# Kernel tuning notes

Measured on AMD Instinct MI355X. Metric: run time of the kernel, lower is better.

The kernel has to match this reference:

```python
import jax, jax.numpy as jnp
import numpy as np

N_NODES = 100000
N_EDGES = 1000000
NEG_SLOPE = 0.2


def gat_conv(x, src, dst, W, al, ar, b, res, activation):
    """DGL-style GATConv. res is None (no residual), 'id' (identity residual), or a [in,H*D] matrix."""
    H, D = al.shape
    n = x.shape[0]
    feat = (x @ W).reshape(n, H, D)                      # [N,H,D]
    el = jnp.einsum('nhd,hd->nh', feat, al)              # [N,H]
    er = jnp.einsum('nhd,hd->nh', feat, ar)              # [N,H]
    e = jax.nn.leaky_relu(el[src] + er[dst], NEG_SLOPE)  # [E,H]
    # edge softmax over incoming edges of each dst node
    m = jax.lax.stop_gradient(jax.ops.segment_max(e, dst, num_segments=n))
    ex = jnp.exp(e - m[dst])
    s = jax.ops.segment_sum(ex, dst, num_segments=n)
    alpha = ex / s[dst]                                  # [E,H]
    out = jax.ops.segment_sum(feat[src] * alpha[:, :, None], dst, num_segments=n)  # [N,H,D]
    if res == 'id':
        out = out + x.reshape(n, H, D)
    elif res is not None:
        out = out + (x @ res).reshape(n, H, D)
    out = out + b.reshape(1, H, D)
    if activation is not None:
        out = activation(out)
    return out


def setup_inputs() -> dict:
    key = jax.random.key(0)
    ks = jax.random.split(key, 20)
    F_IN, HID = 128, 32
    H1, H2, H3 = 4, 4, 1
    C = 40
    sc = 0.1
    inp = {
        'x':   jax.random.normal(ks[0], (N_NODES, F_IN), dtype=jnp.float32),
        'src': jax.random.randint(ks[1], (N_EDGES,), 0, N_NODES, dtype=jnp.int32),
        'dst': jax.random.randint(ks[2], (N_EDGES,), 0, N_NODES, dtype=jnp.int32),
        # layer 1: in=128 -> H1*HID=128, no residual, elu
        'W1':  sc * jax.random.normal(ks[3], (F_IN, H1 * HID), dtype=jnp.float32),
        'al1': sc * jax.random.normal(ks[4], (H1, HID), dtype=jnp.float32),
        'ar1': sc * jax.random.normal(ks[5], (H1, HID), dtype=jnp.float32),
        'b1':  jnp.zeros((H1 * HID,), dtype=jnp.float32),
        # layer 2: in=128 -> H2*HID=128, identity residual, elu
        'W2':  sc * jax.random.normal(ks[6], (H1 * HID, H2 * HID), dtype=jnp.float32),
        'al2': sc * jax.random.normal(ks[7], (H2, HID), dtype=jnp.float32),
        'ar2': sc * jax.random.normal(ks[8], (H2, HID), dtype=jnp.float32),
        'b2':  jnp.zeros((H2 * HID,), dtype=jnp.float32),
        # layer 3 (output): in=128 -> H3*HID=32, projected residual, no activation
        'W3':  sc * jax.random.normal(ks[9], (H2 * HID, H3 * HID), dtype=jnp.float32),
        'al3': sc * jax.random.normal(ks[10], (H3, HID), dtype=jnp.float32),
        'ar3': sc * jax.random.normal(ks[11], (H3, HID), dtype=jnp.float32),
        'b3':  jnp.zeros((H3 * HID,), dtype=jnp.float32),
        'res3': sc * jax.random.normal(ks[12], (H2 * HID, H3 * HID), dtype=jnp.float32),
        # final classifier
        'Wfc': sc * jax.random.normal(ks[13], (HID, C), dtype=jnp.float32),
        'bfc': jnp.zeros((C,), dtype=jnp.float32),
    }
    return inp


def reference(x, src, dst, W1, al1, ar1, b1, W2, al2, ar2, b2, W3, al3, ar3, b3, res3, Wfc, bfc):
    n = x.shape[0]
    h = gat_conv(x, src, dst, W1, al1, ar1, b1, None, jax.nn.elu).reshape(n, -1)   # [N, 128]
    h = gat_conv(h, src, dst, W2, al2, ar2, b2, 'id', jax.nn.elu).reshape(n, -1)   # [N, 128]
    h = gat_conv(h, src, dst, W3, al3, ar3, b3, res3, None).mean(axis=1)           # [N, 32]
    return h @ Wfc + bfc                                                           # [N, 40]
```

## Files before the change

### kernel.cpp

```cpp
#include <hip/hip_runtime.h>
#include <cstdint>
#include <cstddef>

#define NN 100000
#define NE 1000000

typedef unsigned int uint;
typedef unsigned short ushort;
typedef __attribute__((ext_vector_type(8))) short bfrag;
typedef __attribute__((ext_vector_type(4))) float f32x4;

__device__ __forceinline__ ushort f2bf(float f){
  uint u = __float_as_uint(f);
  u += 0x7fffu + ((u >> 16) & 1u);
  return (ushort)(u >> 16);
}
__device__ __forceinline__ float bflo(uint p){ return __uint_as_float(p << 16); }
__device__ __forceinline__ float bfhi(uint p){ return __uint_as_float(p & 0xffff0000u); }


__global__ __launch_bounds__(256) void k_ticket(const int* __restrict__ dst, int* __restrict__ cnt,
                                                int* __restrict__ tick){
  int e = blockIdx.x*256 + threadIdx.x;
  if (e < NE) tick[e] = atomicAdd(&cnt[dst[e]], 1);
}

__global__ __launch_bounds__(256) void k_scan_local(const int* __restrict__ cnt, int* __restrict__ rowptr,
                                                    int* __restrict__ bsum){
  __shared__ int sm[256];
  int t = threadIdx.x;
  int i = blockIdx.x*256 + t;
  int v = (i < NN) ? cnt[i] : 0;
  sm[t] = v;
  __syncthreads();
  for (int off=1; off<256; off<<=1){
    int u = (t>=off) ? sm[t-off] : 0;
    __syncthreads();
    sm[t] += u;
    __syncthreads();
  }
  if (i < NN) rowptr[i] = sm[t] - v;
  if (t == 255) bsum[blockIdx.x] = sm[255];
}

__global__ __launch_bounds__(512) void k_scan_bsum(const int* __restrict__ bsum, int* __restrict__ boff, int nb){
  __shared__ int sm[512];
  int t = threadIdx.x;
  int v = (t < nb) ? bsum[t] : 0;
  sm[t] = v;
  __syncthreads();
  for (int off=1; off<512; off<<=1){
    int u = (t>=off) ? sm[t-off] : 0;
    __syncthreads();
    sm[t] += u;
    __syncthreads();
  }
  if (t < nb) boff[t] = sm[t] - v;
}

__global__ __launch_bounds__(256) void k_scan_add(int* __restrict__ rowptr, const int* __restrict__ boff){
  int i = blockIdx.x*256 + threadIdx.x;
  if (i < NN) rowptr[i] += boff[i>>8];
  else if (i == NN) rowptr[NN] = NE;
}

__global__ __launch_bounds__(256) void k_place(const int* __restrict__ src, const int* __restrict__ dst,
                                               const int* __restrict__ rowptr, const int* __restrict__ tick,
                                               int* __restrict__ csr){
  int e = blockIdx.x*256 + threadIdx.x;
  if (e < NE){
    int d = dst[e];
    csr[rowptr[d] + tick[e]] = src[e];
  }
}


__device__ __forceinline__ void bfrag_body(const float* __restrict__ B1, const float* __restrict__ B2,
                                           int n1, int n2, int NT, ushort* __restrict__ out, int i){
  if (i >= NT*4*64) return;
  int l = i & 63, ks = (i>>6)&3, nt = i>>8;
  int col = nt*16 + (l&15);
  int k0  = ks*32 + (l>>4)*8;
  const float* B; int stride, c;
  if (col < n1){ B = B1; stride = n1; c = col; }
  else         { B = B2; stride = n2; c = col - n1; }
  ushort v[8];
  #pragma unroll
  for (int j=0;j<8;j++) v[j] = f2bf(B[(size_t)(k0+j)*stride + c]);
  uint4 pk;
  pk.x = (uint)v[0] | ((uint)v[1]<<16);
  pk.y = (uint)v[2] | ((uint)v[3]<<16);
  pk.z = (uint)v[4] | ((uint)v[5]<<16);
  pk.w = (uint)v[6] | ((uint)v[7]<<16);
  *(uint4*)(out + (size_t)i*8) = pk;
}

#define CAST_BLOCKS 12500

__global__ __launch_bounds__(256) void k_prep(const float* __restrict__ x, ushort* __restrict__ xb,
                                              const float* __restrict__ W1, const float* __restrict__ W2,
                                              const float* __restrict__ W3, const float* __restrict__ res3,
                                              ushort* __restrict__ Bf1, ushort* __restrict__ Bf2,
                                              ushort* __restrict__ Bf3){
  int bid = blockIdx.x, t = threadIdx.x;
  if (bid < CAST_BLOCKS){
    int i = bid*256 + t;
    float4 v = ((const float4*)x)[i];
    uint2 p;
    p.x = (uint)f2bf(v.x) | ((uint)f2bf(v.y)<<16);
    p.y = (uint)f2bf(v.z) | ((uint)f2bf(v.w)<<16);
    ((uint2*)xb)[i] = p;
  } else {
    int r = bid - CAST_BLOCKS;
    if (r < 8)       bfrag_body(W1, nullptr, 128, 0, 8, Bf1, r*256 + t);
    else if (r < 16) bfrag_body(W2, nullptr, 128, 0, 8, Bf2, (r-8)*256 + t);
    else             bfrag_body(W3, res3,    32, 32, 4, Bf3, (r-16)*256 + t);
  }
}


template<int NT, int NTF, int H>
__global__ __launch_bounds__(256) void k_gemm_mfma(const ushort* __restrict__ Ab, const ushort* __restrict__ Bf,
                                                   ushort* __restrict__ featb, float* __restrict__ Cres,
                                                   const float* __restrict__ al, const float* __restrict__ ar,
                                                   float* __restrict__ el, float* __restrict__ er, int M){
  int t = threadIdx.x;
  int l = t & 63, w = t >> 6;
  int rw = blockIdx.x*64 + w*16;
  int c = l & 15, g = l >> 4;

  f32x4 acc[NT];
  #pragma unroll
  for (int nt=0;nt<NT;nt++) acc[nt] = (f32x4){0.f,0.f,0.f,0.f};

  int rowA = rw + c; if (rowA >= M) rowA = M-1;
  const ushort* Ap = Ab + (size_t)rowA*128 + g*8;
  const bfrag* Bp = (const bfrag*)Bf;

  #pragma unroll
  for (int ks=0; ks<4; ++ks){
    bfrag a = *(const bfrag*)(Ap + ks*32);
    #pragma unroll
    for (int nt=0; nt<NT; ++nt){
      bfrag b = Bp[(nt*4+ks)*64 + l];
      acc[nt] = __builtin_amdgcn_mfma_f32_16x16x32_bf16(a, b, acc[nt], 0, 0, 0);
    }
  }

  float alv[H][2], arv[H][2];
  #pragma unroll
  for (int h=0;h<H;h++){
    alv[h][0]=al[h*32+c];    arv[h][0]=ar[h*32+c];
    alv[h][1]=al[h*32+16+c]; arv[h][1]=ar[h*32+16+c];
  }

  #pragma unroll
  for (int reg=0; reg<4; ++reg){
    int row = rw + g*4 + reg;
    bool ok = row < M;
    #pragma unroll
    for (int h=0;h<H;h++){
      float pl = acc[2*h][reg]*alv[h][0] + acc[2*h+1][reg]*alv[h][1];
      float pr = acc[2*h][reg]*arv[h][0] + acc[2*h+1][reg]*arv[h][1];
      #pragma unroll
      for (int off=1; off<16; off<<=1){ pl += __shfl_xor(pl,off); pr += __shfl_xor(pr,off); }
      if (ok && c==0){ el[(size_t)row*H + h] = pl; er[(size_t)row*H + h] = pr; }
    }
    if (ok){
      #pragma unroll
      for (int nt=0; nt<NTF; ++nt)
        featb[(size_t)row*(NTF*16) + nt*16 + c] = f2bf(acc[nt][reg]);
      #pragma unroll
      for (int nt=NTF; nt<NT; ++nt)
        Cres[(size_t)row*((NT-NTF)*16) + (nt-NTF)*16 + c] = acc[nt][reg];
    }
  }
}


template<int RK, bool OBF>
__global__ __launch_bounds__(256) void k_agg4(const int* __restrict__ rowptr, const int* __restrict__ csr,
                                              const ushort* __restrict__ feat,
                                              const float* __restrict__ el, const float* __restrict__ er,
                                              const void* __restrict__ res, const float* __restrict__ bias,
                                              void* __restrict__ out, int act){
  int lane = threadIdx.x & 63;
  int node = blockIdx.x*4 + (threadIdx.x >> 6);

  int beg = rowptr[node], deg = rowptr[node+1] - beg;

  int l31 = lane & 31;
  int hm  = l31 >> 3;
  int half = lane >> 5;
  float erh = er[(size_t)node*4 + hm];
  const ushort* fbase = feat + (size_t)l31*4;
  const int* cp = csr + beg;

  float ssum = 0.f;
  float a0=0.f, a1=0.f, a2=0.f, a3=0.f;
  int nE = (deg - half + 1) >> 1;

  int i = 0;
  for (; i+4 <= nE; i += 4){
    int e0 = 2*i+half, e1 = e0+2, e2 = e0+4, e3 = e0+6;
    int s0 = cp[e0], s1 = cp[e1], s2 = cp[e2], s3 = cp[e3];
    uint2 p0 = *(const uint2*)(fbase + (size_t)s0*128);
    uint2 p1 = *(const uint2*)(fbase + (size_t)s1*128);
    uint2 p2 = *(const uint2*)(fbase + (size_t)s2*128);
    uint2 p3 = *(const uint2*)(fbase + (size_t)s3*128);
    float v0 = el[(size_t)s0*4+hm] + erh; v0=(v0>0.f)?v0:0.2f*v0; float w0=__expf(v0);
    float v1 = el[(size_t)s1*4+hm] + erh; v1=(v1>0.f)?v1:0.2f*v1; float w1=__expf(v1);
    float v2 = el[(size_t)s2*4+hm] + erh; v2=(v2>0.f)?v2:0.2f*v2; float w2=__expf(v2);
    float v3 = el[(size_t)s3*4+hm] + erh; v3=(v3>0.f)?v3:0.2f*v3; float w3=__expf(v3);
    ssum += w0+w1+w2+w3;
    a0 += w0*bflo(p0.x) + w1*bflo(p1.x) + w2*bflo(p2.x) + w3*bflo(p3.x);
    a1 += w0*bfhi(p0.x) + w1*bfhi(p1.x) + w2*bfhi(p2.x) + w3*bfhi(p3.x);
    a2 += w0*bflo(p0.y) + w1*bflo(p1.y) + w2*bflo(p2.y) + w3*bflo(p3.y);
    a3 += w0*bfhi(p0.y) + w1*bfhi(p1.y) + w2*bfhi(p2.y) + w3*bfhi(p3.y);
  }
  for (; i < nE; ++i){
    int e0 = 2*i+half;
    int s0 = cp[e0];
    uint2 p0 = *(const uint2*)(fbase + (size_t)s0*128);
    float v0 = el[(size_t)s0*4+hm] + erh; v0=(v0>0.f)?v0:0.2f*v0; float w0=__expf(v0);
    ssum += w0;
    a0 += w0*bflo(p0.x); a1 += w0*bfhi(p0.x);
    a2 += w0*bflo(p0.y); a3 += w0*bfhi(p0.y);
  }

  ssum += __shfl_xor(ssum, 32);
  a0 += __shfl_xor(a0, 32); a1 += __shfl_xor(a1, 32);
  a2 += __shfl_xor(a2, 32); a3 += __shfl_xor(a3, 32);
  float inv = (deg > 0) ? 1.f/ssum : 0.f;
  a0 *= inv; a1 *= inv; a2 *= inv; a3 *= inv;

  if (lane < 32){
    float o0=a0, o1=a1, o2=a2, o3=a3;
    if (RK == 1){
      uint2 rv = *(const uint2*)((const ushort*)res + (size_t)node*128 + lane*4);
      o0 += bflo(rv.x); o1 += bfhi(rv.x); o2 += bflo(rv.y); o3 += bfhi(rv.y);
    } else if (RK == 2){
      float4 rv = *(const float4*)((const float*)res + (size_t)node*128 + lane*4);
      o0 += rv.x; o1 += rv.y; o2 += rv.z; o3 += rv.w;
    }
    float4 bv = *(const float4*)(bias + lane*4);
    o0 += bv.x; o1 += bv.y; o2 += bv.z; o3 += bv.w;
    if (act){
      o0 = (o0>0.f)?o0:__expf(o0)-1.f;
      o1 = (o1>0.f)?o1:__expf(o1)-1.f;
      o2 = (o2>0.f)?o2:__expf(o2)-1.f;
      o3 = (o3>0.f)?o3:__expf(o3)-1.f;
    }
    if (OBF){
      uint2 pk;
      pk.x = (uint)f2bf(o0) | ((uint)f2bf(o1)<<16);
      pk.y = (uint)f2bf(o2) | ((uint)f2bf(o3)<<16);
      *(uint2*)((ushort*)out + (size_t)node*128 + lane*4) = pk;
    } else {
      float4 ov; ov.x=o0; ov.y=o1; ov.z=o2; ov.w=o3;
      *(float4*)((float*)out + (size_t)node*128 + lane*4) = ov;
    }
  }
}


__global__ __launch_bounds__(256) void k_agg1(const int* __restrict__ rowptr, const int* __restrict__ csr,
                                              const ushort* __restrict__ feat,
                                              const float* __restrict__ el, const float* __restrict__ er,
                                              const float* __restrict__ res, const float* __restrict__ bias,
                                              float* __restrict__ h3){
  int lane = threadIdx.x & 63;
  int node = blockIdx.x*4 + (threadIdx.x >> 6);

  int beg = rowptr[node], deg = rowptr[node+1] - beg;
  int sub = lane >> 4, fl = lane & 15;
  float er0 = er[node];
  const ushort* fbase = feat + (size_t)fl*2;
  const int* cp = csr + beg;

  float ssum = 0.f, a0 = 0.f, a1 = 0.f;
  for (int ei = sub; ei < deg; ei += 4){
    int s = cp[ei];
    uint pv = *(const uint*)(fbase + (size_t)s*32);
    float v = el[s] + er0; v = (v>0.f)?v:0.2f*v;
    float w = __expf(v);
    ssum += w;
    a0 += w*bflo(pv); a1 += w*bfhi(pv);
  }
  ssum += __shfl_xor(ssum, 16); ssum += __shfl_xor(ssum, 32);
  a0 += __shfl_xor(a0, 16); a0 += __shfl_xor(a0, 32);
  a1 += __shfl_xor(a1, 16); a1 += __shfl_xor(a1, 32);
  float inv = (deg > 0) ? 1.f/ssum : 0.f;

  if (lane < 16){
    float2 rv = *(const float2*)(res + (size_t)node*32 + 2*fl);
    float o0 = a0*inv + rv.x + bias[2*fl];
    float o1 = a1*inv + rv.y + bias[2*fl+1];
    float2 ov; ov.x = o0; ov.y = o1;
    *(float2*)(h3 + (size_t)node*32 + 2*fl) = ov;
  }
}


__global__ __launch_bounds__(256) void k_fc(const float* __restrict__ h, const float* __restrict__ W,
                                            const float* __restrict__ b, float* __restrict__ out){
  __shared__ float Ws[32*40];
  __shared__ float Hs[64][33];
  __shared__ float bs[40];
  int t = threadIdx.x;
  for (int i=t; i<1280; i+=256) Ws[i] = W[i];
  if (t < 40) bs[t] = b[t];
  int n0 = blockIdx.x*64;
  for (int idx=t; idx<512; idx+=256){
    int r = idx>>3, c4 = idx&7;
    float4 v;
    if (n0 + r < NN) v = *(const float4*)(h + (size_t)(n0+r)*32 + c4*4);
    else v = make_float4(0.f,0.f,0.f,0.f);
    Hs[r][c4*4+0]=v.x; Hs[r][c4*4+1]=v.y; Hs[r][c4*4+2]=v.z; Hs[r][c4*4+3]=v.w;
  }
  __syncthreads();
  int n = t>>2, cg = t&3;
  float acc[10];
  #pragma unroll
  for (int j=0;j<10;j++) acc[j] = 0.f;
  #pragma unroll
  for (int k=0;k<32;k++){
    float hv = Hs[n][k];
    #pragma unroll
    for (int j=0;j<10;j++) acc[j] += hv * Ws[k*40 + cg + 4*j];
  }
  int row = n0 + n;
  if (row < NN){
    #pragma unroll
    for (int j=0;j<10;j++) out[(size_t)row*40 + cg + 4*j] = acc[j] + bs[cg+4*j];
  }
}


extern "C" void kernel_launch(void* const* d_in, const int* in_sizes, int n_in,
                              void* d_out, int out_size, void* d_ws, size_t ws_size,
                              hipStream_t stream){
  const float* x    = (const float*)d_in[0];
  const int*   src  = (const int*)  d_in[1];
  const int*   dst  = (const int*)  d_in[2];
  const float* W1   = (const float*)d_in[3];
  const float* al1  = (const float*)d_in[4];
  const float* ar1  = (const float*)d_in[5];
  const float* b1   = (const float*)d_in[6];
  const float* W2   = (const float*)d_in[7];
  const float* al2  = (const float*)d_in[8];
  const float* ar2  = (const float*)d_in[9];
  const float* b2   = (const float*)d_in[10];
  const float* W3   = (const float*)d_in[11];
  const float* al3  = (const float*)d_in[12];
  const float* ar3  = (const float*)d_in[13];
  const float* b3   = (const float*)d_in[14];
  const float* res3 = (const float*)d_in[15];
  const float* Wfc  = (const float*)d_in[16];
  const float* bfc  = (const float*)d_in[17];
  float* out = (float*)d_out;

  char* ws = (char*)d_ws;
  size_t o = 0;
  auto alloc = [&](size_t bytes)->char*{
    char* p = ws + o;
    o += (bytes + 255) & ~(size_t)255;
    return p;
  };
  int*    rowptr = (int*)   alloc((size_t)(NN+1)*4);
  int*    cnt    = (int*)   alloc((size_t)NN*4);
  int*    bsum   = (int*)   alloc(512*4);
  int*    boff   = (int*)   alloc(512*4);
  int*    tick   = (int*)   alloc((size_t)NE*4);
  int*    csr    = (int*)   alloc((size_t)NE*4);
  float*  el     = (float*) alloc((size_t)NN*4*4);
  float*  er     = (float*) alloc((size_t)NN*4*4);
  ushort* xb     = (ushort*)alloc((size_t)NN*128*2);
  ushort* featb  = (ushort*)alloc((size_t)NN*128*2);
  ushort* h1b    = (ushort*)alloc((size_t)NN*128*2);
  ushort* h2b    = (ushort*)alloc((size_t)NN*128*2);
  float*  res3p  = (float*) alloc((size_t)NN*32*4);
  float*  h3     = (float*) alloc((size_t)NN*32*4);
  ushort* Bf1    = (ushort*)alloc((size_t)8*4*64*8*2);
  ushort* Bf2    = (ushort*)alloc((size_t)8*4*64*8*2);
  ushort* Bf3    = (ushort*)alloc((size_t)4*4*64*8*2);
  (void)ws_size; (void)n_in; (void)in_sizes; (void)out_size;

  hipMemsetAsync(cnt, 0, (size_t)NN*4, stream);
  k_ticket<<<(NE+255)/256, 256, 0, stream>>>(dst, cnt, tick);
  int nb = (NN+255)/256;
  k_scan_local<<<nb, 256, 0, stream>>>(cnt, rowptr, bsum);
  k_scan_bsum<<<1, 512, 0, stream>>>(bsum, boff, nb);
  k_scan_add<<<(NN+1+255)/256, 256, 0, stream>>>(rowptr, boff);
  k_place<<<(NE+255)/256, 256, 0, stream>>>(src, dst, rowptr, tick, csr);

  k_prep<<<CAST_BLOCKS+20, 256, 0, stream>>>(x, xb, W1, W2, W3, res3, Bf1, Bf2, Bf3);

  int gemm_blocks = (NN+63)/64;

  k_gemm_mfma<8,8,4><<<gemm_blocks, 256, 0, stream>>>(xb, Bf1, featb, nullptr, al1, ar1, el, er, NN);
  k_agg4<0,true><<<NN/4, 256, 0, stream>>>(rowptr, csr, featb, el, er, nullptr, b1, h1b, 1);

  k_gemm_mfma<8,8,4><<<gemm_blocks, 256, 0, stream>>>(h1b, Bf2, featb, nullptr, al2, ar2, el, er, NN);
  k_agg4<1,true><<<NN/4, 256, 0, stream>>>(rowptr, csr, featb, el, er, h1b, b2, h2b, 1);

  k_gemm_mfma<4,2,1><<<gemm_blocks, 256, 0, stream>>>(h2b, Bf3, featb, res3p, al3, ar3, el, er, NN);
  k_agg1<<<NN/4, 256, 0, stream>>>(rowptr, csr, featb, el, er, res3p, b3, h3);
  k_fc<<<gemm_blocks, 256, 0, stream>>>(h3, Wfc, bfc, out);
}
```

Before: 321.4 us.

## Fuse CSR build into prep/GEMM, widen aggregation gathers, use exp2 softmax

```diff
diff --git a/kernel.cpp b/kernel.cpp
--- a/kernel.cpp
+++ b/kernel.cpp
@@ -4,6 +4,10 @@
 
 #define NN 100000
 #define NE 1000000
+#define GEMM_BLOCKS 1563
+#define TICKET_BLOCKS 3907
+#define CAST_BLOCKS 12500
+#define LOG2E 1.4426950408896340736f
 
 typedef unsigned int uint;
 typedef unsigned short ushort;
@@ -18,12 +22,6 @@
 __device__ __forceinline__ float bflo(uint p){ return __uint_as_float(p << 16); }
 __device__ __forceinline__ float bfhi(uint p){ return __uint_as_float(p & 0xffff0000u); }
 
-
-__global__ __launch_bounds__(256) void k_ticket(const int* __restrict__ dst, int* __restrict__ cnt,
-                                                int* __restrict__ tick){
-  int e = blockIdx.x*256 + threadIdx.x;
-  if (e < NE) tick[e] = atomicAdd(&cnt[dst[e]], 1);
-}
 
 __global__ __launch_bounds__(256) void k_scan_local(const int* __restrict__ cnt, int* __restrict__ rowptr,
                                                     int* __restrict__ bsum){
@@ -64,16 +62,6 @@
   else if (i == NN) rowptr[NN] = NE;
 }
 
-__global__ __launch_bounds__(256) void k_place(const int* __restrict__ src, const int* __restrict__ dst,
-                                               const int* __restrict__ rowptr, const int* __restrict__ tick,
-                                               int* __restrict__ csr){
-  int e = blockIdx.x*256 + threadIdx.x;
-  if (e < NE){
-    int d = dst[e];
-    csr[rowptr[d] + tick[e]] = src[e];
-  }
-}
-
 
 __device__ __forceinline__ void bfrag_body(const float* __restrict__ B1, const float* __restrict__ B2,
                                            int n1, int n2, int NT, ushort* __restrict__ out, int i){
@@ -95,13 +83,13 @@
   *(uint4*)(out + (size_t)i*8) = pk;
 }
 
-#define CAST_BLOCKS 12500
-
 __global__ __launch_bounds__(256) void k_prep(const float* __restrict__ x, ushort* __restrict__ xb,
                                               const float* __restrict__ W1, const float* __restrict__ W2,
                                               const float* __restrict__ W3, const float* __restrict__ res3,
                                               ushort* __restrict__ Bf1, ushort* __restrict__ Bf2,
-                                              ushort* __restrict__ Bf3){
+                                              ushort* __restrict__ Bf3,
+                                              const int* __restrict__ dst, int* __restrict__ cnt,
+                                              int* __restrict__ tick){
   int bid = blockIdx.x, t = threadIdx.x;
   if (bid < CAST_BLOCKS){
     int i = bid*256 + t;
@@ -110,23 +98,26 @@
     p.x = (uint)f2bf(v.x) | ((uint)f2bf(v.y)<<16);
     p.y = (uint)f2bf(v.z) | ((uint)f2bf(v.w)<<16);
     ((uint2*)xb)[i] = p;
-  } else {
+  } else if (bid < CAST_BLOCKS + 20){
     int r = bid - CAST_BLOCKS;
     if (r < 8)       bfrag_body(W1, nullptr, 128, 0, 8, Bf1, r*256 + t);
     else if (r < 16) bfrag_body(W2, nullptr, 128, 0, 8, Bf2, (r-8)*256 + t);
     else             bfrag_body(W3, res3,    32, 32, 4, Bf3, (r-16)*256 + t);
+  } else {
+    int e = (bid - CAST_BLOCKS - 20)*256 + t;
+    if (e < NE) tick[e] = atomicAdd(&cnt[dst[e]], 1);
   }
 }
 
 
 template<int NT, int NTF, int H>
-__global__ __launch_bounds__(256) void k_gemm_mfma(const ushort* __restrict__ Ab, const ushort* __restrict__ Bf,
-                                                   ushort* __restrict__ featb, float* __restrict__ Cres,
-                                                   const float* __restrict__ al, const float* __restrict__ ar,
-                                                   float* __restrict__ el, float* __restrict__ er, int M){
+__device__ __forceinline__ void gemm_body(int bid, const ushort* __restrict__ Ab, const ushort* __restrict__ Bf,
+                                          ushort* __restrict__ featb, float* __restrict__ Cres,
+                                          const float* __restrict__ al, const float* __restrict__ ar,
+                                          float* __restrict__ el, float* __restrict__ er, int M){
   int t = threadIdx.x;
   int l = t & 63, w = t >> 6;
-  int rw = blockIdx.x*64 + w*16;
+  int rw = bid*64 + w*16;
   int c = l & 15, g = l >> 4;
 
   f32x4 acc[NT];
@@ -150,8 +141,8 @@
   float alv[H][2], arv[H][2];
   #pragma unroll
   for (int h=0;h<H;h++){
-    alv[h][0]=al[h*32+c];    arv[h][0]=ar[h*32+c];
-    alv[h][1]=al[h*32+16+c]; arv[h][1]=ar[h*32+16+c];
+    alv[h][0]=al[h*32+c]*LOG2E;    arv[h][0]=ar[h*32+c]*LOG2E;
+    alv[h][1]=al[h*32+16+c]*LOG2E; arv[h][1]=ar[h*32+16+c]*LOG2E;
   }
 
   #pragma unroll
@@ -177,89 +168,122 @@
   }
 }
 
-
-template<int RK, bool OBF>
+template<int NT, int NTF, int H>
+__global__ __launch_bounds__(256) void k_gemm_mfma(const ushort* __restrict__ Ab, const ushort* __restrict__ Bf,
+                                                   ushort* __restrict__ featb, float* __restrict__ Cres,
+                                                   const float* __restrict__ al, const float* __restrict__ ar,
+                                                   float* __restrict__ el, float* __restrict__ er, int M){
+  gemm_body<NT,NTF,H>(blockIdx.x, Ab, Bf, featb, Cres, al, ar, el, er, M);
+}
+
+__global__ __launch_bounds__(256) void k_gemm1_place(const ushort* __restrict__ xb, const ushort* __restrict__ Bf1,
+                                                     ushort* __restrict__ featb,
+                                                     const float* __restrict__ al, const float* __restrict__ ar,
+                                                     float* __restrict__ el, float* __restrict__ er,
+                                                     const int* __restrict__ src, const int* __restrict__ dst,
+                                                     const int* __restrict__ rowptr, const int* __restrict__ tick,
+                                                     int* __restrict__ csr){
+  int bid = blockIdx.x;
+  if (bid < GEMM_BLOCKS){
+    gemm_body<8,8,4>(bid, xb, Bf1, featb, nullptr, al, ar, el, er, NN);
+  } else {
+    int e = (bid - GEMM_BLOCKS)*256 + threadIdx.x;
+    if (e < NE){
+      int d = dst[e];
+      csr[rowptr[d] + tick[e]] = src[e];
+    }
+  }
+}
+
+
+template<int RK>
 __global__ __launch_bounds__(256) void k_agg4(const int* __restrict__ rowptr, const int* __restrict__ csr,
                                               const ushort* __restrict__ feat,
                                               const float* __restrict__ el, const float* __restrict__ er,
                                               const void* __restrict__ res, const float* __restrict__ bias,
-                                              void* __restrict__ out, int act){
+                                              ushort* __restrict__ out, int act){
   int lane = threadIdx.x & 63;
   int node = blockIdx.x*4 + (threadIdx.x >> 6);
 
   int beg = rowptr[node], deg = rowptr[node+1] - beg;
-
-  int l31 = lane & 31;
-  int hm  = l31 >> 3;
-  int half = lane >> 5;
+  int q = lane >> 4, l15 = lane & 15;
+  int hm = l15 >> 2;
   float erh = er[(size_t)node*4 + hm];
-  const ushort* fbase = feat + (size_t)l31*4;
   const int* cp = csr + beg;
+  uint fo = (uint)l15*8u;
 
   float ssum = 0.f;
-  float a0=0.f, a1=0.f, a2=0.f, a3=0.f;
-  int nE = (deg - half + 1) >> 1;
-
-  int i = 0;
-  for (; i+4 <= nE; i += 4){
-    int e0 = 2*i+half, e1 = e0+2, e2 = e0+4, e3 = e0+6;
-    int s0 = cp[e0], s1 = cp[e1], s2 = cp[e2], s3 = cp[e3];
-    uint2 p0 = *(const uint2*)(fbase + (size_t)s0*128);
-    uint2 p1 = *(const uint2*)(fbase + (size_t)s1*128);
-    uint2 p2 = *(const uint2*)(fbase + (size_t)s2*128);
-    uint2 p3 = *(const uint2*)(fbase + (size_t)s3*128);
-    float v0 = el[(size_t)s0*4+hm] + erh; v0=(v0>0.f)?v0:0.2f*v0; float w0=__expf(v0);
-    float v1 = el[(size_t)s1*4+hm] + erh; v1=(v1>0.f)?v1:0.2f*v1; float w1=__expf(v1);
-    float v2 = el[(size_t)s2*4+hm] + erh; v2=(v2>0.f)?v2:0.2f*v2; float w2=__expf(v2);
-    float v3 = el[(size_t)s3*4+hm] + erh; v3=(v3>0.f)?v3:0.2f*v3; float w3=__expf(v3);
-    ssum += w0+w1+w2+w3;
-    a0 += w0*bflo(p0.x) + w1*bflo(p1.x) + w2*bflo(p2.x) + w3*bflo(p3.x);
-    a1 += w0*bfhi(p0.x) + w1*bfhi(p1.x) + w2*bfhi(p2.x) + w3*bfhi(p3.x);
-    a2 += w0*bflo(p0.y) + w1*bflo(p1.y) + w2*bflo(p2.y) + w3*bflo(p3.y);
-    a3 += w0*bfhi(p0.y) + w1*bfhi(p1.y) + w2*bfhi(p2.y) + w3*bfhi(p3.y);
-  }
-  for (; i < nE; ++i){
-    int e0 = 2*i+half;
-    int s0 = cp[e0];
-    uint2 p0 = *(const uint2*)(fbase + (size_t)s0*128);
-    float v0 = el[(size_t)s0*4+hm] + erh; v0=(v0>0.f)?v0:0.2f*v0; float w0=__expf(v0);
+  float a0=0.f,a1=0.f,a2=0.f,a3=0.f,a4=0.f,a5=0.f,a6=0.f,a7=0.f;
+
+  int ei = q;
+  for (; ei + 4 < deg; ei += 8){
+    int s0 = cp[ei], s1 = cp[ei+4];
+    uint4 p0 = *(const uint4*)(feat + ((uint)s0*128u + fo));
+    uint4 p1 = *(const uint4*)(feat + ((uint)s1*128u + fo));
+    float v0 = el[(uint)s0*4u + hm] + erh; v0 = fmaxf(v0, 0.2f*v0);
+    float v1 = el[(uint)s1*4u + hm] + erh; v1 = fmaxf(v1, 0.2f*v1);
+    float w0 = __builtin_amdgcn_exp2f(v0);
+    float w1 = __builtin_amdgcn_exp2f(v1);
+    ssum += w0 + w1;
+    a0 += w0*bflo(p0.x) + w1*bflo(p1.x);
+    a1 += w0*bfhi(p0.x) + w1*bfhi(p1.x);
+    a2 += w0*bflo(p0.y) + w1*bflo(p1.y);
+    a3 += w0*bfhi(p0.y) + w1*bfhi(p1.y);
+    a4 += w0*bflo(p0.z) + w1*bflo(p1.z);
+    a5 += w0*bfhi(p0.z) + w1*bfhi(p1.z);
+    a6 += w0*bflo(p0.w) + w1*bflo(p1.w);
+    a7 += w0*bfhi(p0.w) + w1*bfhi(p1.w);
+  }
+  if (ei < deg){
+    int s0 = cp[ei];
+    uint4 p0 = *(const uint4*)(feat + ((uint)s0*128u + fo));
+    float v0 = el[(uint)s0*4u + hm] + erh; v0 = fmaxf(v0, 0.2f*v0);
+    float w0 = __builtin_amdgcn_exp2f(v0);
     ssum += w0;
     a0 += w0*bflo(p0.x); a1 += w0*bfhi(p0.x);
     a2 += w0*bflo(p0.y); a3 += w0*bfhi(p0.y);
-  }
-
-  ssum += __shfl_xor(ssum, 32);
-  a0 += __shfl_xor(a0, 32); a1 += __shfl_xor(a1, 32);
-  a2 += __shfl_xor(a2, 32); a3 += __shfl_xor(a3, 32);
+    a4 += w0*bflo(p0.z); a5 += w0*bfhi(p0.z);
+    a6 += w0*bflo(p0.w); a7 += w0*bfhi(p0.w);
+  }
+
+  #pragma unroll
+  for (int off=16; off<64; off<<=1){
+    ssum += __shfl_xor(ssum, off);
+    a0 += __shfl_xor(a0, off); a1 += __shfl_xor(a1, off);
+    a2 += __shfl_xor(a2, off); a3 += __shfl_xor(a3, off);
+    a4 += __shfl_xor(a4, off); a5 += __shfl_xor(a5, off);
+    a6 += __shfl_xor(a6, off); a7 += __shfl_xor(a7, off);
+  }
   float inv = (deg > 0) ? 1.f/ssum : 0.f;
-  a0 *= inv; a1 *= inv; a2 *= inv; a3 *= inv;
-
-  if (lane < 32){
-    float o0=a0, o1=a1, o2=a2, o3=a3;
+
+  if (lane < 16){
+    float o0=a0*inv, o1=a1*inv, o2=a2*inv, o3=a3*inv;
+    float o4=a4*inv, o5=a5*inv, o6=a6*inv, o7=a7*inv;
     if (RK == 1){
-      uint2 rv = *(const uint2*)((const ushort*)res + (size_t)node*128 + lane*4);
+      uint4 rv = *(const uint4*)((const ushort*)res + (size_t)node*128 + l15*8);
       o0 += bflo(rv.x); o1 += bfhi(rv.x); o2 += bflo(rv.y); o3 += bfhi(rv.y);
-    } else if (RK == 2){
-      float4 rv = *(const float4*)((const float*)res + (size_t)node*128 + lane*4);
-      o0 += rv.x; o1 += rv.y; o2 += rv.z; o3 += rv.w;
-    }
-    float4 bv = *(const float4*)(bias + lane*4);
-    o0 += bv.x; o1 += bv.y; o2 += bv.z; o3 += bv.w;
+      o4 += bflo(rv.z); o5 += bfhi(rv.z); o6 += bflo(rv.w); o7 += bfhi(rv.w);
+    }
+    float4 bv0 = *(const float4*)(bias + l15*8);
+    float4 bv1 = *(const float4*)(bias + l15*8 + 4);
+    o0 += bv0.x; o1 += bv0.y; o2 += bv0.z; o3 += bv0.w;
+    o4 += bv1.x; o5 += bv1.y; o6 += bv1.z; o7 += bv1.w;
     if (act){
       o0 = (o0>0.f)?o0:__expf(o0)-1.f;
       o1 = (o1>0.f)?o1:__expf(o1)-1.f;
       o2 = (o2>0.f)?o2:__expf(o2)-1.f;
       o3 = (o3>0.f)?o3:__expf(o3)-1.f;
-    }
-    if (OBF){
-      uint2 pk;
-      pk.x = (uint)f2bf(o0) | ((uint)f2bf(o1)<<16);
-      pk.y = (uint)f2bf(o2) | ((uint)f2bf(o3)<<16);
-      *(uint2*)((ushort*)out + (size_t)node*128 + lane*4) = pk;
-    } else {
-      float4 ov; ov.x=o0; ov.y=o1; ov.z=o2; ov.w=o3;
-      *(float4*)((float*)out + (size_t)node*128 + lane*4) = ov;
-    }
+      o4 = (o4>0.f)?o4:__expf(o4)-1.f;
+      o5 = (o5>0.f)?o5:__expf(o5)-1.f;
+      o6 = (o6>0.f)?o6:__expf(o6)-1.f;
+      o7 = (o7>0.f)?o7:__expf(o7)-1.f;
+    }
+    uint4 pk;
+    pk.x = (uint)f2bf(o0) | ((uint)f2bf(o1)<<16);
+    pk.y = (uint)f2bf(o2) | ((uint)f2bf(o3)<<16);
+    pk.z = (uint)f2bf(o4) | ((uint)f2bf(o5)<<16);
+    pk.w = (uint)f2bf(o6) | ((uint)f2bf(o7)<<16);
+    *(uint4*)(out + (size_t)node*128 + l15*8) = pk;
   }
 }
 
@@ -273,31 +297,38 @@
   int node = blockIdx.x*4 + (threadIdx.x >> 6);
 
   int beg = rowptr[node], deg = rowptr[node+1] - beg;
-  int sub = lane >> 4, fl = lane & 15;
+  int sub = lane >> 3, fl = lane & 7;
   float er0 = er[node];
-  const ushort* fbase = feat + (size_t)fl*2;
   const int* cp = csr + beg;
-
-  float ssum = 0.f, a0 = 0.f, a1 = 0.f;
-  for (int ei = sub; ei < deg; ei += 4){
+  uint fo = (uint)fl*4u;
+
+  float ssum = 0.f, a0=0.f, a1=0.f, a2=0.f, a3=0.f;
+  for (int ei = sub; ei < deg; ei += 8){
     int s = cp[ei];
-    uint pv = *(const uint*)(fbase + (size_t)s*32);
-    float v = el[s] + er0; v = (v>0.f)?v:0.2f*v;
-    float w = __expf(v);
+    uint2 pv = *(const uint2*)(feat + ((uint)s*32u + fo));
+    float v = el[s] + er0; v = fmaxf(v, 0.2f*v);
+    float w = __builtin_amdgcn_exp2f(v);
     ssum += w;
-    a0 += w*bflo(pv); a1 += w*bfhi(pv);
-  }
-  ssum += __shfl_xor(ssum, 16); ssum += __shfl_xor(ssum, 32);
-  a0 += __shfl_xor(a0, 16); a0 += __shfl_xor(a0, 32);
-  a1 += __shfl_xor(a1, 16); a1 += __shfl_xor(a1, 32);
+    a0 += w*bflo(pv.x); a1 += w*bfhi(pv.x);
+    a2 += w*bflo(pv.y); a3 += w*bfhi(pv.y);
+  }
+  #pragma unroll
+  for (int off=8; off<64; off<<=1){
+    ssum += __shfl_xor(ssum, off);
+    a0 += __shfl_xor(a0, off); a1 += __shfl_xor(a1, off);
+    a2 += __shfl_xor(a2, off); a3 += __shfl_xor(a3, off);
+  }
   float inv = (deg > 0) ? 1.f/ssum : 0.f;
 
-  if (lane < 16){
-    float2 rv = *(const float2*)(res + (size_t)node*32 + 2*fl);
-    float o0 = a0*inv + rv.x + bias[2*fl];
-    float o1 = a1*inv + rv.y + bias[2*fl+1];
-    float2 ov; ov.x = o0; ov.y = o1;
-    *(float2*)(h3 + (size_t)node*32 + 2*fl) = ov;
+  if (lane < 8){
+    float4 rv = *(const float4*)(res + (size_t)node*32 + fl*4);
+    float4 bv = *(const float4*)(bias + fl*4);
+    float4 ov;
+    ov.x = a0*inv + rv.x + bv.x;
+    ov.y = a1*inv + rv.y + bv.y;
+    ov.z = a2*inv + rv.z + bv.z;
+    ov.w = a3*inv + rv.w + bv.w;
+    *(float4*)(h3 + (size_t)node*32 + fl*4) = ov;
   }
 }
 
@@ -387,24 +418,21 @@
   (void)ws_size; (void)n_in; (void)in_sizes; (void)out_size;
 
   hipMemsetAsync(cnt, 0, (size_t)NN*4, stream);
-  k_ticket<<<(NE+255)/256, 256, 0, stream>>>(dst, cnt, tick);
+  k_prep<<<CAST_BLOCKS+20+TICKET_BLOCKS, 256, 0, stream>>>(x, xb, W1, W2, W3, res3,
+                                                           Bf1, Bf2, Bf3, dst, cnt, tick);
   int nb = (NN+255)/256;
   k_scan_local<<<nb, 256, 0, stream>>>(cnt, rowptr, bsum);
   k_scan_bsum<<<1, 512, 0, stream>>>(bsum, boff, nb);
   k_scan_add<<<(NN+1+255)/256, 256, 0, stream>>>(rowptr, boff);
-  k_place<<<(NE+255)/256, 256, 0, stream>>>(src, dst, rowptr, tick, csr);
-
-  k_prep<<<CAST_BLOCKS+20, 256, 0, stream>>>(x, xb, W1, W2, W3, res3, Bf1, Bf2, Bf3);
-
-  int gemm_blocks = (NN+63)/64;
-
-  k_gemm_mfma<8,8,4><<<gemm_blocks, 256, 0, stream>>>(xb, Bf1, featb, nullptr, al1, ar1, el, er, NN);
-  k_agg4<0,true><<<NN/4, 256, 0, stream>>>(rowptr, csr, featb, el, er, nullptr, b1, h1b, 1);
-
-  k_gemm_mfma<8,8,4><<<gemm_blocks, 256, 0, stream>>>(h1b, Bf2, featb, nullptr, al2, ar2, el, er, NN);
-  k_agg4<1,true><<<NN/4, 256, 0, stream>>>(rowptr, csr, featb, el, er, h1b, b2, h2b, 1);
-
-  k_gemm_mfma<4,2,1><<<gemm_blocks, 256, 0, stream>>>(h2b, Bf3, featb, res3p, al3, ar3, el, er, NN);
+
+  k_gemm1_place<<<GEMM_BLOCKS+TICKET_BLOCKS, 256, 0, stream>>>(xb, Bf1, featb, al1, ar1, el, er,
+                                                               src, dst, rowptr, tick, csr);
+  k_agg4<0><<<NN/4, 256, 0, stream>>>(rowptr, csr, featb, el, er, nullptr, b1, h1b, 1);
+
+  k_gemm_mfma<8,8,4><<<GEMM_BLOCKS, 256, 0, stream>>>(h1b, Bf2, featb, nullptr, al2, ar2, el, er, NN);
+  k_agg4<1><<<NN/4, 256, 0, stream>>>(rowptr, csr, featb, el, er, h1b, b2, h2b, 1);
+
+  k_gemm_mfma<4,2,1><<<GEMM_BLOCKS, 256, 0, stream>>>(h2b, Bf3, featb, res3p, al3, ar3, el, er, NN);
   k_agg1<<<NN/4, 256, 0, stream>>>(rowptr, csr, featb, el, er, res3p, b3, h3);
-  k_fc<<<gemm_blocks, 256, 0, stream>>>(h3, Wfc, bfc, out);
-}
+  k_fc<<<GEMM_BLOCKS, 256, 0, stream>>>(h3, Wfc, bfc, out);
+}
```

Result: faster. 294.2 us (-8.5%).
